# Performance work log

Measured on AMD Instinct MI355X. Metric: run time of the kernel, lower is better.

The kernel has to match this reference:

```python
import jax, jax.numpy as jnp
import numpy as np

B, S, D, H = 4, 1024, 1024, 16
HD = D // H  # 64, even for RoPE


def _rope_tables(seq_len, head_dim):
    inv_freq = 1.0 / (10000.0 ** (jnp.arange(0, head_dim, 2, dtype=jnp.float32) / head_dim))
    pos = jnp.arange(seq_len, dtype=jnp.float32)
    ang = pos[:, None] * inv_freq[None, :]           # [S, HD/2]
    return jnp.cos(ang), jnp.sin(ang)


def _apply_rope(x, cos, sin):
    # x: [B, S, H, HD]; cos/sin: [S, HD/2] broadcast to [1, S, 1, HD/2]
    c = cos[None, :, None, :]
    s = sin[None, :, None, :]
    x1 = x[..., 0::2]
    x2 = x[..., 1::2]
    return jnp.concatenate([x1 * c - x2 * s, x1 * s + x2 * c], axis=-1)


def setup_inputs() -> dict:
    key = jax.random.key(0)
    ks = jax.random.split(key, 11)
    sc = 1.0 / np.sqrt(D)
    inp = {
        "query": jax.random.normal(ks[0], (B, S, D), jnp.float32),
        "key": jax.random.normal(ks[1], (B, S, D), jnp.float32),
        "value": jax.random.normal(ks[2], (B, S, D), jnp.float32),
        "mask": jnp.tril(jnp.ones((S, S), jnp.int32))[None, None],  # causal [1,1,S,S]
        "Wq": jax.random.normal(ks[3], (D, D), jnp.float32) * sc,
        "bq": jnp.zeros((D,), jnp.float32),
        "Wk": jax.random.normal(ks[4], (D, D), jnp.float32) * sc,
        "bk": jnp.zeros((D,), jnp.float32),
        "Wv": jax.random.normal(ks[5], (D, D), jnp.float32) * sc,
        "bv": jnp.zeros((D,), jnp.float32),
        "Wo": jax.random.normal(ks[6], (D, D), jnp.float32) * sc,
        "bo": jnp.zeros((D,), jnp.float32),
    }
    return inp


def reference(query, key, value, mask, Wq, bq, Wk, bk, Wv, bv, Wo, bo):
    Bq, Sq, _ = query.shape
    Sk = key.shape[1]
    q = (query @ Wq + bq).reshape(Bq, Sq, H, HD)
    k = (key @ Wk + bk).reshape(Bq, Sk, H, HD)
    v = (value @ Wv + bv).reshape(Bq, Sk, H, HD)
    cos, sin = _rope_tables(max(Sq, Sk), HD)
    q = _apply_rope(q, cos[:Sq], sin[:Sq])
    k = _apply_rope(k, cos[:Sk], sin[:Sk])
    scores = jnp.einsum("bqhd,bkhd->bhqk", q, k) / jnp.sqrt(jnp.float32(HD))
    scores = jnp.where(mask == 0, jnp.float32(-jnp.inf), scores)
    attn = jax.nn.softmax(scores, axis=-1)  # dropout p=0 (inference)
    ctx = jnp.einsum("bhqk,bkhd->bqhd", attn, v).reshape(Bq, Sq, D)
    return ctx @ Wo + bo
```

## Files before the change

kernel.cpp:

```cpp
#include <hip/hip_runtime.h>
#include <hip/hip_bf16.h>
#include <math.h>

#define B_DIM 4
#define S_DIM 1024
#define D_DIM 1024
#define H_DIM 16
#define HD_DIM 64
#define M_TOT 4096

typedef short short8 __attribute__((ext_vector_type(8)));
typedef float f32x4 __attribute__((ext_vector_type(4)));

__device__ inline float bf2f(short u)
{
    return __uint_as_float(((unsigned)(unsigned short)u) << 16);
}

__device__ inline void gload_lds16(const void* gsrc, void* lds)
{
    __builtin_amdgcn_global_load_lds(
        (const __attribute__((address_space(1))) unsigned int*)gsrc,
        (__attribute__((address_space(3))) unsigned int*)lds, 16, 0, 0);
}

__global__ __launch_bounds__(256) void preamble_kernel(
    const float* __restrict__ W0, const float* __restrict__ W1,
    const float* __restrict__ W2, const float* __restrict__ W3,
    __hip_bfloat16* __restrict__ T0, __hip_bfloat16* __restrict__ T1,
    __hip_bfloat16* __restrict__ T2, __hip_bfloat16* __restrict__ T3,
    float* __restrict__ tab)
{
    const int tid = threadIdx.x;
    if (blockIdx.z == 4) {
        const int fb = blockIdx.y * 32 + blockIdx.x;
        if (fb >= 128) return;
        const int t = fb * 256 + tid;
        const int pos = t >> 5, i = t & 31;
        float inv = powf(10000.0f, -(float)(2 * i) / 64.0f);
        float ang = (float)pos * inv;
        float s, c;
        sincosf(ang, &s, &c);
        tab[t] = c;
        tab[32768 + t] = s;
        return;
    }

    const float* W = (blockIdx.z == 0) ? W0 : (blockIdx.z == 1) ? W1
                    : (blockIdx.z == 2) ? W2 : W3;
    __hip_bfloat16* T = (blockIdx.z == 0) ? T0 : (blockIdx.z == 1) ? T1
                       : (blockIdx.z == 2) ? T2 : T3;

    __shared__ float tile[32][33];
    const int r = tid >> 3;
    const int c4 = (tid & 7) * 4;

    float4 v = *(const float4*)&W[(long)(blockIdx.y * 32 + r) * D_DIM + blockIdx.x * 32 + c4];
    tile[r][c4 + 0] = v.x;
    tile[r][c4 + 1] = v.y;
    tile[r][c4 + 2] = v.z;
    tile[r][c4 + 3] = v.w;
    __syncthreads();

    __hip_bfloat16 o[4];
    o[0] = __float2bfloat16(tile[c4 + 0][r]);
    o[1] = __float2bfloat16(tile[c4 + 1][r]);
    o[2] = __float2bfloat16(tile[c4 + 2][r]);
    o[3] = __float2bfloat16(tile[c4 + 3][r]);
    *(uint2*)&T[(long)(blockIdx.x * 32 + r) * D_DIM + blockIdx.y * 32 + c4] = *(uint2*)o;
}

__global__ __launch_bounds__(256, 3) void gemm_qkv_kernel(
    const float* __restrict__ Xq, const float* __restrict__ Xk,
    const float* __restrict__ Xv,
    const __hip_bfloat16* __restrict__ WtQ, const __hip_bfloat16* __restrict__ WtK,
    const __hip_bfloat16* __restrict__ WtV,
    const float* __restrict__ bq, const float* __restrict__ bk,
    const float* __restrict__ bv,
    __hip_bfloat16* __restrict__ Qo, __hip_bfloat16* __restrict__ Ko,
    __hip_bfloat16* __restrict__ Vto)
{
    __shared__ __align__(16) __hip_bfloat16 Al[128][40];
    __shared__ __align__(16) __hip_bfloat16 Bl[128][32];

    const int F = blockIdx.x + 8 * blockIdx.y + 256 * blockIdx.z;
    const int xcd = F & 7;
    const int sb = F >> 3;
    const int z = sb >> 5;
    const int n0 = (sb & 7) * 128;
    const int m0 = ((xcd << 2) | ((sb >> 3) & 3)) * 128;

    const float* X = (z == 0) ? Xq : (z == 1) ? Xk : Xv;
    const __hip_bfloat16* Wt = (z == 0) ? WtQ : (z == 1) ? WtK : WtV;
    const float* bias = (z == 0) ? bq : (z == 1) ? bk : bv;

    const int tid = threadIdx.x;
    const int l = tid & 63;
    const int w = tid >> 6;

    const int srow = w * 16 + (l >> 2);
    const int skc = (l & 3) * 8;
    const __hip_bfloat16* Bbase = Wt + (long)(n0 + srow) * D_DIM + skc;
    char* ldsB0 = (char*)&Bl[0][0] + w * 1024;

    const int arow = tid >> 1;
    const int ak = (tid & 1) * 16;
    const float* Af = X + (long)(m0 + arow) * D_DIM + ak;

    const int lrow = l & 15;
    const int kg = l >> 4;
    const int wr = (w >> 1) * 64;
    const int wc = (w & 1) * 64;

    f32x4 acc[4][4];
#pragma unroll
    for (int i = 0; i < 4; ++i)
#pragma unroll
        for (int j = 0; j < 4; ++j) acc[i][j] = (f32x4){0.f, 0.f, 0.f, 0.f};

    float4 f0 = *(const float4*)(Af);
    float4 f1 = *(const float4*)(Af + 4);
    float4 f2 = *(const float4*)(Af + 8);
    float4 f3 = *(const float4*)(Af + 12);

    for (int k0 = 0; k0 < D_DIM; k0 += 32) {
        float fa[16] = {f0.x, f0.y, f0.z, f0.w, f1.x, f1.y, f1.z, f1.w,
                        f2.x, f2.y, f2.z, f2.w, f3.x, f3.y, f3.z, f3.w};
        __attribute__((aligned(16))) __hip_bfloat16 ab[16];
#pragma unroll
        for (int i = 0; i < 16; ++i) ab[i] = __float2bfloat16(fa[i]);

        __syncthreads();
        *(short8*)&Al[arow][ak]     = ((const short8*)ab)[0];
        *(short8*)&Al[arow][ak + 8] = ((const short8*)ab)[1];
        gload_lds16(Bbase + k0, ldsB0);
        gload_lds16(Bbase + 64 * D_DIM + k0, ldsB0 + 4096);
        __syncthreads();

        if (k0 + 32 < D_DIM) {
            f0 = *(const float4*)(Af + k0 + 32);
            f1 = *(const float4*)(Af + k0 + 36);
            f2 = *(const float4*)(Af + k0 + 40);
            f3 = *(const float4*)(Af + k0 + 44);
        }

        short8 af[4], bf[4];
#pragma unroll
        for (int i = 0; i < 4; ++i)
            af[i] = *(const short8*)&Al[wr + i * 16 + lrow][kg * 8];
#pragma unroll
        for (int j = 0; j < 4; ++j)
            bf[j] = *(const short8*)&Bl[wc + j * 16 + lrow][kg * 8];
#pragma unroll
        for (int i = 0; i < 4; ++i)
#pragma unroll
            for (int j = 0; j < 4; ++j)
                acc[i][j] = __builtin_amdgcn_mfma_f32_16x16x32_bf16(
                    af[i], bf[j], acc[i][j], 0, 0, 0);
    }

#pragma unroll
    for (int i = 0; i < 4; ++i) {
#pragma unroll
        for (int j = 0; j < 4; ++j) {
            const int col = n0 + wc + j * 16 + lrow;
            const float bvs = bias[col];
            const int rbase = m0 + wr + i * 16 + kg * 4;
            if (z < 2) {
                __hip_bfloat16* Out = (z == 0) ? Qo : Ko;
#pragma unroll
                for (int r = 0; r < 4; ++r)
                    Out[(long)(rbase + r) * D_DIM + col] =
                        __float2bfloat16(acc[i][j][r] + bvs);
            } else {
                const int hh = col >> 6, dd = col & 63;
                const int bb = rbase >> 10, s0 = rbase & 1023;
                __hip_bfloat16 o[4];
#pragma unroll
                for (int r = 0; r < 4; ++r)
                    o[r] = __float2bfloat16(acc[i][j][r] + bvs);
                *(uint2*)&Vto[((long)((bb * H_DIM + hh) * HD_DIM + dd)) * S_DIM + s0] =
                    *(uint2*)o;
            }
        }
    }
}

__global__ __launch_bounds__(256, 2) void gemm_wo_kernel(
    const __hip_bfloat16* __restrict__ X, const __hip_bfloat16* __restrict__ Wt,
    const float* __restrict__ bias, float* __restrict__ Out)
{
    __shared__ __align__(16) __hip_bfloat16 Al[128][32];
    __shared__ __align__(16) __hip_bfloat16 Bl[64][32];

    const int F = blockIdx.x;
    const int xcd = F & 7;
    const int s = F >> 3;
    const int n0 = (s & 15) * 64;
    const int m0 = ((xcd << 2) | (s >> 4)) * 128;

    const int tid = threadIdx.x;
    const int l = tid & 63;
    const int w = tid >> 6;

    const int srow = w * 16 + (l >> 2);
    const int skc = (l & 3) * 8;
    const __hip_bfloat16* Abase = X + (long)(m0 + srow) * D_DIM + skc;
    const __hip_bfloat16* Bbase = Wt + (long)(n0 + srow) * D_DIM + skc;
    char* ldsA0 = (char*)&Al[0][0] + w * 1024;
    char* ldsB0 = (char*)&Bl[0][0] + w * 1024;

    const int lrow = l & 15;
    const int kg = l >> 4;
    const int wr = (w >> 1) * 64;
    const int wc = (w & 1) * 32;

    f32x4 acc[4][2];
#pragma unroll
    for (int i = 0; i < 4; ++i)
#pragma unroll
        for (int j = 0; j < 2; ++j) acc[i][j] = (f32x4){0.f, 0.f, 0.f, 0.f};

    for (int k0 = 0; k0 < D_DIM; k0 += 32) {
        __syncthreads();
        gload_lds16(Abase + k0, ldsA0);
        gload_lds16(Abase + 64 * D_DIM + k0, ldsA0 + 4096);
        gload_lds16(Bbase + k0, ldsB0);
        __syncthreads();

        short8 af[4], bf[2];
#pragma unroll
        for (int i = 0; i < 4; ++i)
            af[i] = *(const short8*)&Al[wr + i * 16 + lrow][kg * 8];
#pragma unroll
        for (int j = 0; j < 2; ++j)
            bf[j] = *(const short8*)&Bl[wc + j * 16 + lrow][kg * 8];
#pragma unroll
        for (int i = 0; i < 4; ++i)
#pragma unroll
            for (int j = 0; j < 2; ++j)
                acc[i][j] = __builtin_amdgcn_mfma_f32_16x16x32_bf16(
                    af[i], bf[j], acc[i][j], 0, 0, 0);
    }

#pragma unroll
    for (int i = 0; i < 4; ++i) {
#pragma unroll
        for (int j = 0; j < 2; ++j) {
            const int col = n0 + wc + j * 16 + lrow;
            const float bv = bias[col];
            const int rbase = m0 + wr + i * 16 + kg * 4;
#pragma unroll
            for (int r = 0; r < 4; ++r)
                Out[(long)(rbase + r) * D_DIM + col] = acc[i][j][r] + bv;
        }
    }
}

__global__ __launch_bounds__(256) void rope_bf16_kernel(
    const __hip_bfloat16* __restrict__ Qi, const __hip_bfloat16* __restrict__ Ki,
    __hip_bfloat16* __restrict__ Qo, __hip_bfloat16* __restrict__ Ko,
    const float* __restrict__ tab)
{
    const long t = (long)blockIdx.x * 256 + threadIdx.x;
    const int row = (int)(t >> 7);
    const int slot = (int)(t & 127);
    const int hh = slot >> 3;
    const int p0 = (slot & 7) * 4;
    const int pos = row & (S_DIM - 1);
    const bool isQ = (blockIdx.y == 0);
    const float scale = isQ ? 0.125f : 1.0f;

    const __hip_bfloat16* src = (isQ ? Qi : Ki) + (long)row * D_DIM + hh * HD_DIM;
    __hip_bfloat16* dst = (isQ ? Qo : Ko) + (long)row * D_DIM + hh * HD_DIM;

    short8 xv = *(const short8*)&src[2 * p0];
    float4 cv = *(const float4*)&tab[pos * 32 + p0];
    float4 sv = *(const float4*)&tab[32768 + pos * 32 + p0];
    float cc[4] = {cv.x, cv.y, cv.z, cv.w};
    float ss[4] = {sv.x, sv.y, sv.z, sv.w};

    __hip_bfloat16 o1[4], o2[4];
#pragma unroll
    for (int j = 0; j < 4; ++j) {
        float x1 = bf2f(xv[2 * j]);
        float x2 = bf2f(xv[2 * j + 1]);
        o1[j] = __float2bfloat16((x1 * cc[j] - x2 * ss[j]) * scale);
        o2[j] = __float2bfloat16((x1 * ss[j] + x2 * cc[j]) * scale);
    }
    *(uint2*)&dst[p0]      = *(uint2*)o1;
    *(uint2*)&dst[p0 + 32] = *(uint2*)o2;
}

#define KPAD 72

__global__ __launch_bounds__(256, 2) void attn_mfma_kernel(
    const __hip_bfloat16* __restrict__ Q,
    const __hip_bfloat16* __restrict__ K,
    const __hip_bfloat16* __restrict__ Vt,
    __hip_bfloat16* __restrict__ CTX)
{
    __shared__ __align__(16) __hip_bfloat16 Kl[64][KPAD];
    __shared__ __align__(16) __hip_bfloat16 Vl[64][KPAD];
    __shared__ __align__(16) __hip_bfloat16 Pl[4][32][KPAD];
    __shared__ __align__(16) float aS[4][2][16];

    const int tid = threadIdx.x;
    const int l = tid & 63;
    const int w = tid >> 6;

    const int bid = blockIdx.x + 8 * blockIdx.y + 128 * blockIdx.z;
    const int half = bid >> 8;
    const int idx = bid & 255;
    int qt = idx & 7;
    if (half) qt = 7 - qt;
    const int rest = idx >> 3;
    const int h = rest & 15;
    const int b = (rest >> 4) | (half << 1);

    const int lrow = l & 15;
    const int kg = l >> 4;
    const int kg4 = kg * 4;

    const int q0w = qt * 128 + w * 32;
    const long qrow_base = (long)b * S_DIM + q0w;

    short8 qf[2][2];
#pragma unroll
    for (int m = 0; m < 2; ++m)
#pragma unroll
        for (int ks = 0; ks < 2; ++ks)
            qf[m][ks] = *(const short8*)&Q[(qrow_base + m * 16 + lrow) * D_DIM +
                                           h * HD_DIM + ks * 32 + kg * 8];

    f32x4 ctx[2][4];
#pragma unroll
    for (int m = 0; m < 2; ++m)
#pragma unroll
        for (int d = 0; d < 4; ++d) ctx[m][d] = (f32x4){0.f, 0.f, 0.f, 0.f};
    float mrun[2] = {-1e30f, -1e30f};
    float lrun[2] = {0.f, 0.f};

    const int sr = tid >> 2;
    const int sc2 = (tid & 3) * 16;
    const __hip_bfloat16* Kg = K + ((long)b * S_DIM + sr) * D_DIM + h * HD_DIM + sc2;
    const __hip_bfloat16* Vg = Vt + ((long)((b * H_DIM + h) * HD_DIM) + sr) * S_DIM + sc2;

    const int ktmax = 2 * qt + 1;

    short8 kp0 = *(const short8*)Kg;
    short8 kp1 = *(const short8*)(Kg + 8);
    short8 vp0 = *(const short8*)Vg;
    short8 vp1 = *(const short8*)(Vg + 8);

    for (int kt = 0; kt <= ktmax; ++kt) {
        __syncthreads();
        *(short8*)&Kl[sr][sc2]     = kp0;
        *(short8*)&Kl[sr][sc2 + 8] = kp1;
        *(short8*)&Vl[sr][sc2]     = vp0;
        *(short8*)&Vl[sr][sc2 + 8] = vp1;
        if (kt < ktmax) {
            const __hip_bfloat16* kp = Kg + (long)(kt + 1) * 64 * D_DIM;
            const __hip_bfloat16* vp = Vg + (kt + 1) * 64;
            kp0 = *(const short8*)kp;
            kp1 = *(const short8*)(kp + 8);
            vp0 = *(const short8*)vp;
            vp1 = *(const short8*)(vp + 8);
        }
        __syncthreads();

        if (kt * 64 > q0w + 31) continue;

        f32x4 sac[2][4];
#pragma unroll
        for (int m = 0; m < 2; ++m)
#pragma unroll
            for (int nt = 0; nt < 4; ++nt) sac[m][nt] = (f32x4){0.f, 0.f, 0.f, 0.f};

        short8 kf[4][2];
#pragma unroll
        for (int nt = 0; nt < 4; ++nt)
#pragma unroll
            for (int ks = 0; ks < 2; ++ks)
                kf[nt][ks] = *(const short8*)&Kl[nt * 16 + lrow][ks * 32 + kg * 8];
#pragma unroll
        for (int m = 0; m < 2; ++m)
#pragma unroll
            for (int nt = 0; nt < 4; ++nt)
#pragma unroll
                for (int ks = 0; ks < 2; ++ks)
                    sac[m][nt] = __builtin_amdgcn_mfma_f32_16x16x32_bf16(
                        kf[nt][ks], qf[m][ks], sac[m][nt], 0, 0, 0);

        const bool partial = (kt * 64 + 63 > q0w);
        const int kbase = kt * 64;
#pragma unroll
        for (int m = 0; m < 2; ++m) {
            const int qg = q0w + m * 16 + lrow;
            float s[16];
#pragma unroll
            for (int nt = 0; nt < 4; ++nt)
#pragma unroll
                for (int r = 0; r < 4; ++r) {
                    float v = sac[m][nt][r];
                    if (partial && (kbase + nt * 16 + kg4 + r > qg)) v = -1e30f;
                    s[nt * 4 + r] = v;
                }
            float t8[8];
#pragma unroll
            for (int i = 0; i < 8; ++i) t8[i] = fmaxf(s[i], s[i + 8]);
#pragma unroll
            for (int i = 0; i < 4; ++i) t8[i] = fmaxf(t8[i], t8[i + 4]);
            float mx = fmaxf(fmaxf(t8[0], t8[1]), fmaxf(t8[2], t8[3]));
            mx = fmaxf(mx, __shfl_xor(mx, 16));
            mx = fmaxf(mx, __shfl_xor(mx, 32));
            const float mnew = fmaxf(mrun[m], mx);
            const float alpha = __expf(mrun[m] - mnew);
            mrun[m] = mnew;

            float p0s = 0.f, p1s = 0.f, p2s = 0.f, p3s = 0.f;
            __attribute__((aligned(8))) __hip_bfloat16 pb[16];
#pragma unroll
            for (int i = 0; i < 4; ++i) {
                float p = __expf(s[i] - mnew);      p0s += p; pb[i] = __float2bfloat16(p);
            }
#pragma unroll
            for (int i = 4; i < 8; ++i) {
                float p = __expf(s[i] - mnew);      p1s += p; pb[i] = __float2bfloat16(p);
            }
#pragma unroll
            for (int i = 8; i < 12; ++i) {
                float p = __expf(s[i] - mnew);      p2s += p; pb[i] = __float2bfloat16(p);
            }
#pragma unroll
            for (int i = 12; i < 16; ++i) {
                float p = __expf(s[i] - mnew);      p3s += p; pb[i] = __float2bfloat16(p);
            }
            float sum = (p0s + p1s) + (p2s + p3s);
            sum += __shfl_xor(sum, 16);
            sum += __shfl_xor(sum, 32);
            lrun[m] = lrun[m] * alpha + sum;

            if (kg == 0) aS[w][m][lrow] = alpha;
#pragma unroll
            for (int nt = 0; nt < 4; ++nt)
                *(uint2*)&Pl[w][m * 16 + lrow][nt * 16 + kg4] = *(uint2*)&pb[nt * 4];
        }

#pragma unroll
        for (int m = 0; m < 2; ++m) {
            f32x4 al4 = *(const f32x4*)&aS[w][m][kg4];
#pragma unroll
            for (int dt = 0; dt < 4; ++dt)
#pragma unroll
                for (int r = 0; r < 4; ++r) ctx[m][dt][r] *= al4[r];
        }

        short8 vf[4][2];
#pragma unroll
        for (int dt = 0; dt < 4; ++dt)
#pragma unroll
            for (int ks = 0; ks < 2; ++ks)
                vf[dt][ks] = *(const short8*)&Vl[dt * 16 + lrow][ks * 32 + kg * 8];
#pragma unroll
        for (int m = 0; m < 2; ++m) {
            short8 pf[2];
#pragma unroll
            for (int ks = 0; ks < 2; ++ks)
                pf[ks] = *(const short8*)&Pl[w][m * 16 + lrow][ks * 32 + kg * 8];
#pragma unroll
            for (int dt = 0; dt < 4; ++dt)
#pragma unroll
                for (int ks = 0; ks < 2; ++ks)
                    ctx[m][dt] = __builtin_amdgcn_mfma_f32_16x16x32_bf16(
                        pf[ks], vf[dt][ks], ctx[m][dt], 0, 0, 0);
        }
    }

    if (kg == 0) {
        aS[w][0][lrow] = lrun[0];
        aS[w][1][lrow] = lrun[1];
    }
#pragma unroll
    for (int m = 0; m < 2; ++m) {
        f32x4 lv = *(const f32x4*)&aS[w][m][kg4];
#pragma unroll
        for (int r = 0; r < 4; ++r) {
            const float inv_l = 1.0f / lv[r];
            const long rowoff = (qrow_base + m * 16 + kg4 + r) * D_DIM + h * HD_DIM;
#pragma unroll
            for (int dt = 0; dt < 4; ++dt)
                CTX[rowoff + dt * 16 + lrow] = __float2bfloat16(ctx[m][dt][r] * inv_l);
        }
    }
}

extern "C" void kernel_launch(void* const* d_in, const int* in_sizes, int n_in,
                              void* d_out, int out_size, void* d_ws, size_t ws_size,
                              hipStream_t stream)
{
    const float* query = (const float*)d_in[0];
    const float* key   = (const float*)d_in[1];
    const float* value = (const float*)d_in[2];
    const float* Wq = (const float*)d_in[4];
    const float* bq = (const float*)d_in[5];
    const float* Wk = (const float*)d_in[6];
    const float* bk = (const float*)d_in[7];
    const float* Wv = (const float*)d_in[8];
    const float* bv = (const float*)d_in[9];
    const float* Wo = (const float*)d_in[10];
    const float* bo = (const float*)d_in[11];

    char* wsb = (char*)d_ws;
    __hip_bfloat16* Qw    = (__hip_bfloat16*)(wsb);
    __hip_bfloat16* Kw    = (__hip_bfloat16*)(wsb + (8L  << 20));
    __hip_bfloat16* Vtb   = (__hip_bfloat16*)(wsb + (16L << 20));
    __hip_bfloat16* Qr    = (__hip_bfloat16*)(wsb + (24L << 20));
    __hip_bfloat16* Kr    = (__hip_bfloat16*)(wsb + (32L << 20));
    __hip_bfloat16* CTXbf = (__hip_bfloat16*)(wsb + (40L << 20));
    __hip_bfloat16* WtQ   = (__hip_bfloat16*)(wsb + (48L << 20));
    __hip_bfloat16* WtK   = (__hip_bfloat16*)(wsb + (50L << 20));
    __hip_bfloat16* WtV   = (__hip_bfloat16*)(wsb + (52L << 20));
    __hip_bfloat16* WtO   = (__hip_bfloat16*)(wsb + (54L << 20));
    float*          tab   = (float*)(wsb + (56L << 20));

    preamble_kernel<<<dim3(32, 32, 5), 256, 0, stream>>>(
        Wq, Wk, Wv, Wo, WtQ, WtK, WtV, WtO, tab);

    gemm_qkv_kernel<<<dim3(8, 32, 3), 256, 0, stream>>>(
        query, key, value, WtQ, WtK, WtV, bq, bk, bv, Qw, Kw, Vtb);

    rope_bf16_kernel<<<dim3(2048, 2), 256, 0, stream>>>(Qw, Kw, Qr, Kr, tab);

    attn_mfma_kernel<<<dim3(8, 16, 4), 256, 0, stream>>>(Qr, Kr, Vtb, CTXbf);

    gemm_wo_kernel<<<512, 256, 0, stream>>>(CTXbf, WtO, bo, (float*)d_out);
}
```

Measured before the change: 112.0 us.

## Double-buffer LDS tiles in QKV projection GEMM with one barrier per step

Splits the QKV projection GEMM's A and B shared-memory tiles into two buffers. The next K-slice's weight load (global-to-LDS) and bf16-converted activations are written into the alternate buffer while MFMAs run on the current one. Manual s_waitcnt plus a single s_barrier per iteration replace the two __syncthreads. This overlaps global memory latency with compute but doubles LDS use, which may lower occupancy, and depends on hand-written waitcnt counts being correct.

```diff
diff --git a/kernel.cpp b/kernel.cpp
--- a/kernel.cpp
+++ b/kernel.cpp
@@ -80,8 +80,8 @@
     __hip_bfloat16* __restrict__ Qo, __hip_bfloat16* __restrict__ Ko,
     __hip_bfloat16* __restrict__ Vto)
 {
-    __shared__ __align__(16) __hip_bfloat16 Al[128][40];
-    __shared__ __align__(16) __hip_bfloat16 Bl[128][32];
+    __shared__ __align__(16) __hip_bfloat16 Al[2][128][40];
+    __shared__ __align__(16) __hip_bfloat16 Bl[2][128][32];
 
     const int F = blockIdx.x + 8 * blockIdx.y + 256 * blockIdx.z;
     const int xcd = F & 7;
@@ -101,7 +101,8 @@
     const int srow = w * 16 + (l >> 2);
     const int skc = (l & 3) * 8;
     const __hip_bfloat16* Bbase = Wt + (long)(n0 + srow) * D_DIM + skc;
-    char* ldsB0 = (char*)&Bl[0][0] + w * 1024;
+    char* ldsB0 = (char*)&Bl[0][0][0] + w * 1024;
+    char* ldsB1 = (char*)&Bl[1][0][0] + w * 1024;
 
     const int arow = tid >> 1;
     const int ak = (tid & 1) * 16;
@@ -118,45 +119,80 @@
 #pragma unroll
         for (int j = 0; j < 4; ++j) acc[i][j] = (f32x4){0.f, 0.f, 0.f, 0.f};
 
-    float4 f0 = *(const float4*)(Af);
-    float4 f1 = *(const float4*)(Af + 4);
-    float4 f2 = *(const float4*)(Af + 8);
-    float4 f3 = *(const float4*)(Af + 12);
-
-    for (int k0 = 0; k0 < D_DIM; k0 += 32) {
+    float4 f0, f1, f2, f3;
+
+    {
+        f0 = *(const float4*)(Af);
+        f1 = *(const float4*)(Af + 4);
+        f2 = *(const float4*)(Af + 8);
+        f3 = *(const float4*)(Af + 12);
         float fa[16] = {f0.x, f0.y, f0.z, f0.w, f1.x, f1.y, f1.z, f1.w,
                         f2.x, f2.y, f2.z, f2.w, f3.x, f3.y, f3.z, f3.w};
         __attribute__((aligned(16))) __hip_bfloat16 ab[16];
 #pragma unroll
         for (int i = 0; i < 16; ++i) ab[i] = __float2bfloat16(fa[i]);
-
-        __syncthreads();
-        *(short8*)&Al[arow][ak]     = ((const short8*)ab)[0];
-        *(short8*)&Al[arow][ak + 8] = ((const short8*)ab)[1];
-        gload_lds16(Bbase + k0, ldsB0);
-        gload_lds16(Bbase + 64 * D_DIM + k0, ldsB0 + 4096);
-        __syncthreads();
-
-        if (k0 + 32 < D_DIM) {
-            f0 = *(const float4*)(Af + k0 + 32);
-            f1 = *(const float4*)(Af + k0 + 36);
-            f2 = *(const float4*)(Af + k0 + 40);
-            f3 = *(const float4*)(Af + k0 + 44);
+        *(short8*)&Al[0][arow][ak]     = ((const short8*)ab)[0];
+        *(short8*)&Al[0][arow][ak + 8] = ((const short8*)ab)[1];
+        gload_lds16(Bbase, ldsB0);
+        gload_lds16(Bbase + 64 * D_DIM, ldsB0 + 4096);
+        asm volatile("" ::: "memory");
+        f0 = *(const float4*)(Af + 32);
+        f1 = *(const float4*)(Af + 36);
+        f2 = *(const float4*)(Af + 40);
+        f3 = *(const float4*)(Af + 44);
+        asm volatile("s_waitcnt vmcnt(4)" ::: "memory");
+        asm volatile("s_waitcnt lgkmcnt(0)" ::: "memory");
+        __builtin_amdgcn_s_barrier();
+    }
+
+    for (int t = 0; t < 32; ++t) {
+        const int p = t & 1;
+        const int q = p ^ 1;
+        char* ldsBq = (q == 0) ? ldsB0 : ldsB1;
+
+        if (t < 31) {
+            const int k1 = (t + 1) * 32;
+            gload_lds16(Bbase + k1, ldsBq);
+            gload_lds16(Bbase + 64 * D_DIM + k1, ldsBq + 4096);
+            float fa[16] = {f0.x, f0.y, f0.z, f0.w, f1.x, f1.y, f1.z, f1.w,
+                            f2.x, f2.y, f2.z, f2.w, f3.x, f3.y, f3.z, f3.w};
+            __attribute__((aligned(16))) __hip_bfloat16 ab[16];
+#pragma unroll
+            for (int i = 0; i < 16; ++i) ab[i] = __float2bfloat16(fa[i]);
+            *(short8*)&Al[q][arow][ak]     = ((const short8*)ab)[0];
+            *(short8*)&Al[q][arow][ak + 8] = ((const short8*)ab)[1];
+        }
+        asm volatile("" ::: "memory");
+        if (t < 30) {
+            const int k2 = (t + 2) * 32;
+            f0 = *(const float4*)(Af + k2);
+            f1 = *(const float4*)(Af + k2 + 4);
+            f2 = *(const float4*)(Af + k2 + 8);
+            f3 = *(const float4*)(Af + k2 + 12);
         }
 
         short8 af[4], bf[4];
 #pragma unroll
         for (int i = 0; i < 4; ++i)
-            af[i] = *(const short8*)&Al[wr + i * 16 + lrow][kg * 8];
+            af[i] = *(const short8*)&Al[p][wr + i * 16 + lrow][kg * 8];
 #pragma unroll
         for (int j = 0; j < 4; ++j)
-            bf[j] = *(const short8*)&Bl[wc + j * 16 + lrow][kg * 8];
+            bf[j] = *(const short8*)&Bl[p][wc + j * 16 + lrow][kg * 8];
 #pragma unroll
         for (int i = 0; i < 4; ++i)
 #pragma unroll
             for (int j = 0; j < 4; ++j)
                 acc[i][j] = __builtin_amdgcn_mfma_f32_16x16x32_bf16(
                     af[i], bf[j], acc[i][j], 0, 0, 0);
+
+        if (t < 31) {
+            if (t < 30)
+                asm volatile("s_waitcnt vmcnt(4)" ::: "memory");
+            else
+                asm volatile("s_waitcnt vmcnt(0)" ::: "memory");
+            asm volatile("s_waitcnt lgkmcnt(0)" ::: "memory");
+            __builtin_amdgcn_s_barrier();
+        }
     }
 
 #pragma unroll
```

After: 110.9 us, median of 3. No clear change (-1.0%).
